# Kernel optimization log

Hardware: AMD Instinct MI355X
Metric: run time of the kernel (lower is better)

Reference implementation:

```python
import jax, jax.numpy as jnp
import numpy as np

B, C, F_, T = 32, 2, 1024, 512
CF = C * F_
H = 128  # lstm hidden / embedding dim


def setup_inputs() -> dict:
    key = jax.random.key(0)
    ks = jax.random.split(key, 12)
    s = 0.05
    return {
        "x": jax.random.normal(ks[0], (B, C, F_, T), dtype=jnp.float32),
        "W_fc1": jax.random.normal(ks[1], (H, CF), dtype=jnp.float32) * s,
        "b_fc1": jax.random.normal(ks[2], (H,), dtype=jnp.float32) * s,
        "Wih_f": jax.random.normal(ks[3], (4 * H, H), dtype=jnp.float32) * s,
        "Whh_f": jax.random.normal(ks[4], (4 * H, H), dtype=jnp.float32) * s,
        "b_f": jax.random.normal(ks[5], (4 * H,), dtype=jnp.float32) * s,
        "Wih_b": jax.random.normal(ks[6], (4 * H, H), dtype=jnp.float32) * s,
        "Whh_b": jax.random.normal(ks[7], (4 * H, H), dtype=jnp.float32) * s,
        "b_b": jax.random.normal(ks[8], (4 * H,), dtype=jnp.float32) * s,
        "W_out": jax.random.normal(ks[9], (H, 2 * H), dtype=jnp.float32) * s,
        "b_out": jax.random.normal(ks[10], (H,), dtype=jnp.float32) * s,
    }


def _lstm_scan(x, Wih, Whh, b):
    # x: (L, T, H); recurrence over L (torch treats the (B,128) input as an
    # unbatched sequence of length B), vectorized over the T frames.
    L, Tn, _ = x.shape
    Hn = Whh.shape[1]

    def step(carry, xt):
        h, c = carry  # (T, H)
        z = xt @ Wih.T + h @ Whh.T + b  # (T, 4H)
        i, f, g, o = jnp.split(z, 4, axis=-1)
        c = jax.nn.sigmoid(f) * c + jax.nn.sigmoid(i) * jnp.tanh(g)
        h = jax.nn.sigmoid(o) * jnp.tanh(c)
        return (h, c), h

    init = (jnp.zeros((Tn, Hn), x.dtype), jnp.zeros((Tn, Hn), x.dtype))
    _, hs = jax.lax.scan(step, init, x)
    return hs  # (L, T, H)


def reference(x, W_fc1, b_fc1, Wih_f, Whh_f, b_f, Wih_b, Whh_b, b_b, W_out, b_out):
    Bn, Cn, Fn, Tn = x.shape
    # fc1 applied per time frame: (B, CF, T) -> (B, T, 128)
    xr = x.reshape(Bn, Cn * Fn, Tn).transpose(0, 2, 1)
    h = jnp.einsum("btc,dc->btd", xr, W_fc1) + b_fc1
    # bidirectional LSTM over the batch axis (torch unbatched-input semantics)
    hf = _lstm_scan(h, Wih_f, Whh_f, b_f)
    hb = _lstm_scan(h[::-1], Wih_b, Whh_b, b_b)[::-1]
    hs = jnp.concatenate([hf, hb], axis=-1)  # (B, T, 256)
    out = jnp.einsum("btd,ed->bte", hs, W_out) + b_out  # (B, T, 128)
    return out.transpose(0, 2, 1)  # (B, 128, T), matching torch.stack(dim=2)
```

## Files before the change

### kernel.cpp

```cpp
#include <hip/hip_runtime.h>
#include <stdint.h>

typedef __attribute__((ext_vector_type(8))) short short8;
typedef __attribute__((ext_vector_type(4))) float floatx4;

__device__ __forceinline__ float bf16_to_f(uint16_t u) {
    union { uint32_t i; float f; } v; v.i = ((uint32_t)u) << 16; return v.f;
}
__device__ __forceinline__ uint16_t f_to_bf16(float f) {
    union { uint32_t i; float f; } v; v.f = f;
    uint32_t u = v.i;
    u += 0x7FFFu + ((u >> 16) & 1u);
    return (uint16_t)(u >> 16);
}
__device__ __forceinline__ void gload16(const void* g, void* l) {
    __builtin_amdgcn_global_load_lds(
        (const __attribute__((address_space(1))) void*)g,
        (__attribute__((address_space(3))) void*)l, 16, 0, 0);
}
__device__ __forceinline__ float rcpf(float x) { return __builtin_amdgcn_rcpf(x); }

#define B_  32
#define T_  512
#define CF_ 2048
#define H_  128
#define G4_ 512
#define LOG2E 1.4426950408889634f

__global__ __launch_bounds__(256) void k_cvt_all(
        const float* __restrict__ Wfc, const float* __restrict__ Wih_f,
        const float* __restrict__ Wih_b, const float* __restrict__ Whh_f,
        const float* __restrict__ Whh_b, const float* __restrict__ Wout,
        uint16_t* __restrict__ WfcB, uint16_t* __restrict__ WihB,
        uint16_t* __restrict__ WhhB, uint16_t* __restrict__ WoutB) {
    const int blk = blockIdx.x;
    const float* s; uint16_t* d; int off;
    if (blk < 256)      { s = Wfc;   d = WfcB;          off = blk; }
    else if (blk < 320) { s = Wih_f; d = WihB;          off = blk - 256; }
    else if (blk < 384) { s = Wih_b; d = WihB + 65536;  off = blk - 320; }
    else if (blk < 448) { s = Whh_f; d = WhhB;          off = blk - 384; }
    else if (blk < 512) { s = Whh_b; d = WhhB + 65536;  off = blk - 448; }
    else                { s = Wout;  d = WoutB;         off = blk - 512; }
    const int i = off * 1024 + threadIdx.x * 4;
    float4 v = *(const float4*)&s[i];
    ushort4 o;
    o.x = f_to_bf16(v.x); o.y = f_to_bf16(v.y);
    o.z = f_to_bf16(v.z); o.w = f_to_bf16(v.w);
    *(ushort4*)&d[i] = o;
}

__global__ __launch_bounds__(512) void k_fc1x(const float* __restrict__ x,
                                              const uint16_t* __restrict__ WfcB,
                                              const float* __restrict__ bfc,
                                              const uint16_t* __restrict__ WihB,
                                              const float* __restrict__ b_f,
                                              const float* __restrict__ b_b,
                                              uint16_t* __restrict__ Xp) {
    __shared__ float tile[32 * 65];
    __shared__ __align__(16) uint16_t As[8192];
    __shared__ __align__(16) uint16_t Bs[2176];
    __shared__ __align__(16) uint16_t Hs2[4352];

    const int bb = blockIdx.y, n0 = blockIdx.x * 32;
    const int tid = threadIdx.x, w = tid >> 6, l = tid & 63;
    const int lm = l & 15, lk = l >> 4;
    const float* xb = x + (size_t)bb * CF_ * T_;

    const int t4 = (tid & 7) * 4, cf_r = tid >> 3;
    const int kk = (tid & 15) * 4, t_r = tid >> 4;

    float4 xv = *(const float4*)&xb[(size_t)cf_r * T_ + n0 + t4];

    const int dw = w * 16;
    floatx4 acc[2] = {};
    for (int k0 = 0; k0 < CF_; k0 += 64) {
        __syncthreads();
        tile[(t4 + 0) * 65 + cf_r] = xv.x;
        tile[(t4 + 1) * 65 + cf_r] = xv.y;
        tile[(t4 + 2) * 65 + cf_r] = xv.z;
        tile[(t4 + 3) * 65 + cf_r] = xv.w;
        gload16(WfcB + (size_t)l * CF_ + k0 + w * 8,        As + (w * 128 + l) * 8);
        gload16(WfcB + (size_t)(64 + l) * CF_ + k0 + w * 8, As + (w * 128 + 64 + l) * 8);
        __syncthreads();
        if (k0 + 64 < CF_)
            xv = *(const float4*)&xb[(size_t)(k0 + 64 + cf_r) * T_ + n0 + t4];
        {
            ushort4 o;
            o.x = f_to_bf16(tile[t_r * 65 + kk + 0]);
            o.y = f_to_bf16(tile[t_r * 65 + kk + 1]);
            o.z = f_to_bf16(tile[t_r * 65 + kk + 2]);
            o.w = f_to_bf16(tile[t_r * 65 + kk + 3]);
            *(ushort4*)&Bs[((kk >> 3) * 34 + t_r) * 8 + (kk & 7)] = o;
        }
        __syncthreads();
        short8 a[2], bfr[2][2];
        #pragma unroll
        for (int kf = 0; kf < 2; ++kf) {
            a[kf] = *(const short8*)&As[((kf * 4 + lk) * 128 + dw + lm) * 8];
            #pragma unroll
            for (int nf = 0; nf < 2; ++nf)
                bfr[nf][kf] = *(const short8*)&Bs[((kf * 4 + lk) * 34 + nf * 16 + lm) * 8];
        }
        #pragma unroll
        for (int nf = 0; nf < 2; ++nf) {
            acc[nf] = __builtin_amdgcn_mfma_f32_16x16x32_bf16(a[0], bfr[nf][0], acc[nf], 0, 0, 0);
            acc[nf] = __builtin_amdgcn_mfma_f32_16x16x32_bf16(a[1], bfr[nf][1], acc[nf], 0, 0, 0);
        }
    }
    __syncthreads();
    {
        const int d0 = dw + lk * 4;
        const float4 bv = *(const float4*)&bfc[d0];
        const int c = d0 >> 3;
        #pragma unroll
        for (int nf = 0; nf < 2; ++nf) {
            const int t = nf * 16 + lm;
            ushort4 o;
            o.x = f_to_bf16(acc[nf][0] + bv.x);
            o.y = f_to_bf16(acc[nf][1] + bv.y);
            o.z = f_to_bf16(acc[nf][2] + bv.z);
            o.w = f_to_bf16(acc[nf][3] + bv.w);
            *(ushort4*)&Hs2[(c * 34 + t) * 8 + (lk & 1) * 4] = o;
        }
    }
    __syncthreads();

    const int dirw = w >> 2;
    const int db   = dirw * B_ + bb;
    const uint16_t* Wp = WihB + (size_t)dirw * (G4_ * H_);
    const float* bi = dirw ? b_b : b_f;
    #pragma unroll
    for (int it = 0; it < 2; ++it) {
        const int gbase = (w & 3) * 64 + it * 256;
        short8 aw[4][4];
        #pragma unroll
        for (int mf = 0; mf < 4; ++mf)
            #pragma unroll
            for (int kf = 0; kf < 4; ++kf)
                aw[mf][kf] = *(const short8*)&Wp[(size_t)(gbase + mf * 16 + lm) * H_ + kf * 32 + lk * 8];
        short8 bbf[4];
        floatx4 acc2[4][2] = {};
        #pragma unroll
        for (int nf = 0; nf < 2; ++nf) {
            #pragma unroll
            for (int kf = 0; kf < 4; ++kf)
                bbf[kf] = *(const short8*)&Hs2[((kf * 4 + lk) * 34 + nf * 16 + lm) * 8];
            #pragma unroll
            for (int mf = 0; mf < 4; ++mf)
                #pragma unroll
                for (int kf = 0; kf < 4; ++kf)
                    acc2[mf][nf] = __builtin_amdgcn_mfma_f32_16x16x32_bf16(aw[mf][kf], bbf[kf], acc2[mf][nf], 0, 0, 0);
        }
        #pragma unroll
        for (int mf = 0; mf < 4; ++mf) {
            const int g0 = gbase + mf * 16 + lk * 4;
            const float4 bv = *(const float4*)&bi[g0];
            #pragma unroll
            for (int nf = 0; nf < 2; ++nf) {
                const int t = n0 + nf * 16 + lm;
                ushort4 o;
                o.x = f_to_bf16(acc2[mf][nf][0] + bv.x);
                o.y = f_to_bf16(acc2[mf][nf][1] + bv.y);
                o.z = f_to_bf16(acc2[mf][nf][2] + bv.z);
                o.w = f_to_bf16(acc2[mf][nf][3] + bv.w);
                *(ushort4*)&Xp[((size_t)db * T_ + t) * G4_ + g0] = o;
            }
        }
    }
}

__global__ __launch_bounds__(512) void k_lstm(const uint16_t* __restrict__ Xp,
                                              const uint16_t* __restrict__ WhhB,
                                              uint16_t* __restrict__ hs) {
    __shared__ __align__(16) uint16_t h_sh[16 * 136];
    __shared__ float z_sh[16 * 516];
    const int dir = blockIdx.y, t0 = blockIdx.x * 16;
    const int tid = threadIdx.x, w = tid >> 6, l = tid & 63;
    const int lm = l & 15, lk = l >> 4;
    const int gw = w * 64;
    const uint16_t* Wp = WhhB + dir * (G4_ * H_);

    short8 bw[4][4];
    #pragma unroll
    for (int nf = 0; nf < 4; ++nf)
        #pragma unroll
        for (int kf = 0; kf < 4; ++kf)
            bw[nf][kf] = *(const short8*)&Wp[(size_t)(gw + nf * 16 + lm) * H_ + kf * 32 + lk * 8];

    for (int i = tid; i < 16 * 136; i += 512) h_sh[i] = 0;
    const int hh = tid & 127, tq = tid >> 7;
    float c[4] = {0.f, 0.f, 0.f, 0.f};
    __syncthreads();

    for (int s = 0; s < 32; ++s) {
        const int b_idx = dir ? (31 - s) : s;
        const uint16_t* xp = Xp + ((size_t)(dir * B_ + b_idx) * T_ + t0) * G4_;
        uint16_t xv[4][4];
        #pragma unroll
        for (int j = 0; j < 4; ++j)
            #pragma unroll
            for (int gg = 0; gg < 4; ++gg)
                xv[j][gg] = xp[(size_t)(tq * 4 + j) * G4_ + gg * H_ + hh];

        short8 af[4];
        #pragma unroll
        for (int kf = 0; kf < 4; ++kf)
            af[kf] = *(const short8*)&h_sh[lm * 136 + kf * 32 + lk * 8];
        floatx4 acc[4] = {};
        #pragma unroll
        for (int nf = 0; nf < 4; ++nf)
            #pragma unroll
            for (int kf = 0; kf < 4; ++kf)
                acc[nf] = __builtin_amdgcn_mfma_f32_16x16x32_bf16(af[kf], bw[nf][kf], acc[nf], 0, 0, 0);
        #pragma unroll
        for (int nf = 0; nf < 4; ++nf)
            #pragma unroll
            for (int r = 0; r < 4; ++r)
                z_sh[(lk * 4 + r) * 516 + gw + nf * 16 + lm] = acc[nf][r];
        __syncthreads();

        #pragma unroll
        for (int j = 0; j < 4; ++j) {
            const int t = tq * 4 + j;
            const float* zr = &z_sh[t * 516];
            float zi = zr[hh]            + bf16_to_f(xv[j][0]);
            float zf = zr[H_ + hh]       + bf16_to_f(xv[j][1]);
            float zg = zr[2 * H_ + hh]   + bf16_to_f(xv[j][2]);
            float zo = zr[3 * H_ + hh]   + bf16_to_f(xv[j][3]);
            float si = rcpf(1.f + __builtin_amdgcn_exp2f(-LOG2E * zi));
            float sf = rcpf(1.f + __builtin_amdgcn_exp2f(-LOG2E * zf));
            float so = rcpf(1.f + __builtin_amdgcn_exp2f(-LOG2E * zo));
            float tg = 1.f - 2.f * rcpf(1.f + __builtin_amdgcn_exp2f(2.f * LOG2E * zg));
            c[j] = sf * c[j] + si * tg;
            float tc = 1.f - 2.f * rcpf(1.f + __builtin_amdgcn_exp2f(2.f * LOG2E * c[j]));
            float hn = so * tc;
            uint16_t hb = f_to_bf16(hn);
            h_sh[t * 136 + hh] = hb;
            hs[((size_t)b_idx * T_ + t0 + t) * 256 + dir * H_ + hh] = hb;
        }
        __syncthreads();
    }
}

__global__ __launch_bounds__(256) void k_outm(const uint16_t* __restrict__ WoutB,
                                              const uint16_t* __restrict__ hs,
                                              const float* __restrict__ bout,
                                              float* __restrict__ out) {
    __shared__ __align__(16) uint16_t As[4096], Bs[4096];
    const int b = blockIdx.z, m0 = blockIdx.y * 64, n0 = blockIdx.x * 64;
    const int tid = threadIdx.x, w = tid >> 6, l = tid & 63;
    const int wm = (w >> 1) * 32, wn = (w & 1) * 32;
    const int lm = l & 15, lk = l >> 4;
    const uint16_t* gA = WoutB + (size_t)(m0 + l) * 256;
    const uint16_t* gB = hs + ((size_t)b * T_ + n0 + l) * 256;
    floatx4 acc[2][2] = {};
    for (int k0 = 0; k0 < 256; k0 += 64) {
        __syncthreads();
        gload16(gA + k0 + (2 * w) * 8,     As + ((2 * w) * 64 + l) * 8);
        gload16(gA + k0 + (2 * w + 1) * 8, As + ((2 * w + 1) * 64 + l) * 8);
        gload16(gB + k0 + (2 * w) * 8,     Bs + ((2 * w) * 64 + l) * 8);
        gload16(gB + k0 + (2 * w + 1) * 8, Bs + ((2 * w + 1) * 64 + l) * 8);
        __syncthreads();
        short8 a[2][2], bfr[2][2];
        #pragma unroll
        for (int kf = 0; kf < 2; ++kf) {
            #pragma unroll
            for (int mf = 0; mf < 2; ++mf)
                a[mf][kf] = *(const short8*)&As[((kf * 4 + lk) * 64 + wm + mf * 16 + lm) * 8];
            #pragma unroll
            for (int nf = 0; nf < 2; ++nf)
                bfr[nf][kf] = *(const short8*)&Bs[((kf * 4 + lk) * 64 + wn + nf * 16 + lm) * 8];
        }
        #pragma unroll
        for (int mf = 0; mf < 2; ++mf)
            #pragma unroll
            for (int nf = 0; nf < 2; ++nf) {
                acc[mf][nf] = __builtin_amdgcn_mfma_f32_16x16x32_bf16(a[mf][0], bfr[nf][0], acc[mf][nf], 0, 0, 0);
                acc[mf][nf] = __builtin_amdgcn_mfma_f32_16x16x32_bf16(a[mf][1], bfr[nf][1], acc[mf][nf], 0, 0, 0);
            }
    }
    #pragma unroll
    for (int mf = 0; mf < 2; ++mf) {
        const int e0 = m0 + wm + mf * 16 + lk * 4;
        const float4 bv = *(const float4*)&bout[e0];
        #pragma unroll
        for (int nf = 0; nf < 2; ++nf) {
            const int t = n0 + wn + nf * 16 + lm;
            out[((size_t)b * H_ + e0 + 0) * T_ + t] = acc[mf][nf][0] + bv.x;
            out[((size_t)b * H_ + e0 + 1) * T_ + t] = acc[mf][nf][1] + bv.y;
            out[((size_t)b * H_ + e0 + 2) * T_ + t] = acc[mf][nf][2] + bv.z;
            out[((size_t)b * H_ + e0 + 3) * T_ + t] = acc[mf][nf][3] + bv.w;
        }
    }
}

extern "C" void kernel_launch(void* const* d_in, const int* in_sizes, int n_in,
                              void* d_out, int out_size, void* d_ws, size_t ws_size,
                              hipStream_t stream) {
    const float* x     = (const float*)d_in[0];
    const float* Wfc   = (const float*)d_in[1];
    const float* bfc   = (const float*)d_in[2];
    const float* Wih_f = (const float*)d_in[3];
    const float* Whh_f = (const float*)d_in[4];
    const float* b_f   = (const float*)d_in[5];
    const float* Wih_b = (const float*)d_in[6];
    const float* Whh_b = (const float*)d_in[7];
    const float* b_b   = (const float*)d_in[8];
    const float* Wout  = (const float*)d_in[9];
    const float* bout  = (const float*)d_in[10];
    float* out = (float*)d_out;

    char* ws = (char*)d_ws;
    uint16_t* Xp    = (uint16_t*)(ws);
    uint16_t* hsB   = (uint16_t*)(ws + 33554432);
    uint16_t* WfcB  = (uint16_t*)(ws + 41943040);
    uint16_t* WihB  = (uint16_t*)(ws + 42467328);
    uint16_t* WhhB  = (uint16_t*)(ws + 42729472);
    uint16_t* WoutB = (uint16_t*)(ws + 42991616);

    k_cvt_all<<<dim3(544), 256, 0, stream>>>(Wfc, Wih_f, Wih_b, Whh_f, Whh_b, Wout,
                                             WfcB, WihB, WhhB, WoutB);
    k_fc1x <<<dim3(16, 32),  512, 0, stream>>>(x, WfcB, bfc, WihB, b_f, b_b, Xp);
    k_lstm <<<dim3(32, 2),   512, 0, stream>>>(Xp, WhhB, hsB);
    k_outm <<<dim3(8, 2, 32), 256, 0, stream>>>(WoutB, hsB, bout, out);
}
```

Baseline: 306.7 us.

## Split fc1 GEMM over K into four partial blocks with separate reduction kernel

The fc1 projection now runs as a split-K GEMM: the K dimension is divided into four chunks, giving four times as many blocks (2048 instead of 512). Each block writes fp32 partial sums to a workspace buffer. A new kernel sums the partials, adds the bias and then does the Wih input projection that the old fused kernel performed. The goal is better occupancy on the bandwidth-bound fc1 pass, at the cost of an extra launch and about 32MB of partial-sum traffic.

Result: slower. 327.5 us (+6.8%).

```diff
diff --git a/kernel.cpp b/kernel.cpp
--- a/kernel.cpp
+++ b/kernel.cpp
@@ -49,19 +49,15 @@
     *(ushort4*)&d[i] = o;
 }
 
-__global__ __launch_bounds__(512) void k_fc1x(const float* __restrict__ x,
+__global__ __launch_bounds__(512) void k_fc1p(const float* __restrict__ x,
                                               const uint16_t* __restrict__ WfcB,
-                                              const float* __restrict__ bfc,
-                                              const uint16_t* __restrict__ WihB,
-                                              const float* __restrict__ b_f,
-                                              const float* __restrict__ b_b,
-                                              uint16_t* __restrict__ Xp) {
+                                              float* __restrict__ P) {
     __shared__ float tile[32 * 65];
     __shared__ __align__(16) uint16_t As[8192];
     __shared__ __align__(16) uint16_t Bs[2176];
-    __shared__ __align__(16) uint16_t Hs2[4352];
 
     const int bb = blockIdx.y, n0 = blockIdx.x * 32;
+    const int k_base = blockIdx.z * 512;
     const int tid = threadIdx.x, w = tid >> 6, l = tid & 63;
     const int lm = l & 15, lk = l >> 4;
     const float* xb = x + (size_t)bb * CF_ * T_;
@@ -69,21 +65,21 @@
     const int t4 = (tid & 7) * 4, cf_r = tid >> 3;
     const int kk = (tid & 15) * 4, t_r = tid >> 4;
 
-    float4 xv = *(const float4*)&xb[(size_t)cf_r * T_ + n0 + t4];
+    float4 xv = *(const float4*)&xb[(size_t)(k_base + cf_r) * T_ + n0 + t4];
 
     const int dw = w * 16;
     floatx4 acc[2] = {};
-    for (int k0 = 0; k0 < CF_; k0 += 64) {
+    for (int k0 = 0; k0 < 512; k0 += 64) {
         __syncthreads();
         tile[(t4 + 0) * 65 + cf_r] = xv.x;
         tile[(t4 + 1) * 65 + cf_r] = xv.y;
         tile[(t4 + 2) * 65 + cf_r] = xv.z;
         tile[(t4 + 3) * 65 + cf_r] = xv.w;
-        gload16(WfcB + (size_t)l * CF_ + k0 + w * 8,        As + (w * 128 + l) * 8);
-        gload16(WfcB + (size_t)(64 + l) * CF_ + k0 + w * 8, As + (w * 128 + 64 + l) * 8);
-        __syncthreads();
-        if (k0 + 64 < CF_)
-            xv = *(const float4*)&xb[(size_t)(k0 + 64 + cf_r) * T_ + n0 + t4];
+        gload16(WfcB + (size_t)l * CF_ + k_base + k0 + w * 8,        As + (w * 128 + l) * 8);
+        gload16(WfcB + (size_t)(64 + l) * CF_ + k_base + k0 + w * 8, As + (w * 128 + 64 + l) * 8);
+        __syncthreads();
+        if (k0 + 64 < 512)
+            xv = *(const float4*)&xb[(size_t)(k_base + k0 + 64 + cf_r) * T_ + n0 + t4];
         {
             ushort4 o;
             o.x = f_to_bf16(tile[t_r * 65 + kk + 0]);
@@ -107,21 +103,46 @@
             acc[nf] = __builtin_amdgcn_mfma_f32_16x16x32_bf16(a[1], bfr[nf][1], acc[nf], 0, 0, 0);
         }
     }
-    __syncthreads();
+    const int d0 = dw + lk * 4;
+    #pragma unroll
+    for (int nf = 0; nf < 2; ++nf) {
+        const int t = n0 + nf * 16 + lm;
+        float4 o = {acc[nf][0], acc[nf][1], acc[nf][2], acc[nf][3]};
+        *(float4*)&P[((size_t)(blockIdx.z * B_ + bb) * T_ + t) * H_ + d0] = o;
+    }
+}
+
+__global__ __launch_bounds__(512) void k_fc1r(const float* __restrict__ P,
+                                              const float* __restrict__ bfc,
+                                              const uint16_t* __restrict__ WihB,
+                                              const float* __restrict__ b_f,
+                                              const float* __restrict__ b_b,
+                                              uint16_t* __restrict__ Xp) {
+    __shared__ __align__(16) uint16_t Hs2[4352];
+    const int bb = blockIdx.y, n0 = blockIdx.x * 32;
+    const int tid = threadIdx.x, w = tid >> 6, l = tid & 63;
+    const int lm = l & 15, lk = l >> 4;
+
     {
-        const int d0 = dw + lk * 4;
-        const float4 bv = *(const float4*)&bfc[d0];
-        const int c = d0 >> 3;
-        #pragma unroll
-        for (int nf = 0; nf < 2; ++nf) {
-            const int t = nf * 16 + lm;
-            ushort4 o;
-            o.x = f_to_bf16(acc[nf][0] + bv.x);
-            o.y = f_to_bf16(acc[nf][1] + bv.y);
-            o.z = f_to_bf16(acc[nf][2] + bv.z);
-            o.w = f_to_bf16(acc[nf][3] + bv.w);
-            *(ushort4*)&Hs2[(c * 34 + t) * 8 + (lk & 1) * 4] = o;
-        }
+        const int t = tid >> 4, d8 = (tid & 15) * 8;
+        float4 s0 = {0.f, 0.f, 0.f, 0.f}, s1 = {0.f, 0.f, 0.f, 0.f};
+        #pragma unroll
+        for (int ks = 0; ks < 4; ++ks) {
+            const float* p = &P[((size_t)(ks * B_ + bb) * T_ + n0 + t) * H_ + d8];
+            float4 a = *(const float4*)p;
+            float4 b = *(const float4*)(p + 4);
+            s0.x += a.x; s0.y += a.y; s0.z += a.z; s0.w += a.w;
+            s1.x += b.x; s1.y += b.y; s1.z += b.z; s1.w += b.w;
+        }
+        const float4 bv0 = *(const float4*)&bfc[d8];
+        const float4 bv1 = *(const float4*)&bfc[d8 + 4];
+        ushort4 o0, o1;
+        o0.x = f_to_bf16(s0.x + bv0.x); o0.y = f_to_bf16(s0.y + bv0.y);
+        o0.z = f_to_bf16(s0.z + bv0.z); o0.w = f_to_bf16(s0.w + bv0.w);
+        o1.x = f_to_bf16(s1.x + bv1.x); o1.y = f_to_bf16(s1.y + bv1.y);
+        o1.z = f_to_bf16(s1.z + bv1.z); o1.w = f_to_bf16(s1.w + bv1.w);
+        *(ushort4*)&Hs2[((d8 >> 3) * 34 + t) * 8] = o0;
+        *(ushort4*)&Hs2[((d8 >> 3) * 34 + t) * 8 + 4] = o1;
     }
     __syncthreads();
 
@@ -317,10 +338,12 @@
     uint16_t* WihB  = (uint16_t*)(ws + 42467328);
     uint16_t* WhhB  = (uint16_t*)(ws + 42729472);
     uint16_t* WoutB = (uint16_t*)(ws + 42991616);
+    float*    P     = (float*)   (ws + 43057152);
 
     k_cvt_all<<<dim3(544), 256, 0, stream>>>(Wfc, Wih_f, Wih_b, Whh_f, Whh_b, Wout,
                                              WfcB, WihB, WhhB, WoutB);
-    k_fc1x <<<dim3(16, 32),  512, 0, stream>>>(x, WfcB, bfc, WihB, b_f, b_b, Xp);
-    k_lstm <<<dim3(32, 2),   512, 0, stream>>>(Xp, WhhB, hsB);
-    k_outm <<<dim3(8, 2, 32), 256, 0, stream>>>(WoutB, hsB, bout, out);
-}
+    k_fc1p <<<dim3(16, 32, 4), 512, 0, stream>>>(x, WfcB, P);
+    k_fc1r <<<dim3(16, 32),    512, 0, stream>>>(P, bfc, WihB, b_f, b_b, Xp);
+    k_lstm <<<dim3(32, 2),     512, 0, stream>>>(Xp, WhhB, hsB);
+    k_outm <<<dim3(8, 2, 32),  256, 0, stream>>>(WoutB, hsB, bout, out);
+}
```
